# Performance work log

Hardware: AMD Instinct MI355X
Metric: run time of the kernel (lower is better)

## Reference

```python
import jax, jax.numpy as jnp
import numpy as np

DIM = 256
NUM_HEADS = 8
HEAD_DIM = DIM // NUM_HEADS


def setup_inputs() -> dict:
    key = jax.random.key(0)
    k1, k2, k3, k4 = jax.random.split(key, 4)
    B, C, H, W = 16, DIM, 64, 64
    x = jax.random.normal(k1, (B, C, H, W), dtype=jnp.float32)
    # 1x1 convs as dense weight matrices [out_ch, in_ch]
    Wqkv = jax.random.normal(k2, (3 * DIM, DIM), dtype=jnp.float32) * (DIM ** -0.5)
    Wproj = jax.random.normal(k3, (DIM, DIM), dtype=jnp.float32) * (DIM ** -0.5)
    bproj = jax.random.normal(k4, (DIM,), dtype=jnp.float32) * 0.01
    return {"x": x, "Wqkv": Wqkv, "Wproj": Wproj, "bproj": bproj}


def reference(x, Wqkv, Wproj, bproj):
    B, C, H, W = x.shape
    N = H * W
    hd = C // NUM_HEADS

    # qkv: 1x1 conv (no bias) == channel matmul
    qkv = jnp.einsum('oc,bchw->bohw', Wqkv, x)  # [B, 3C, H, W]
    q, k, v = jnp.split(qkv, 3, axis=1)

    def to_heads(t):
        # b (h d) x y -> b h (x y) d
        return t.reshape(B, NUM_HEADS, hd, N).transpose(0, 1, 3, 2)

    q, k, v = to_heads(q), to_heads(k), to_heads(v)  # [B, h, N, d]

    # linear attention feature map + per-token normalization over d
    q = jax.nn.elu(q) + 1.0
    k = jax.nn.elu(k) + 1.0
    q = q / jnp.sum(q, axis=-1, keepdims=True)
    k = k / jnp.sum(k, axis=-1, keepdims=True)

    kv = jnp.einsum('bhnd,bhne->bhde', k, v)   # [B, h, d, d]
    out = jnp.einsum('bhnd,bhde->bhne', q, kv)  # [B, h, N, d]

    # b h (x y) d -> b (h d) x y
    out = out.transpose(0, 1, 3, 2).reshape(B, C, H, W)

    # proj: 1x1 conv with bias; drop_path is identity in eval mode
    out = jnp.einsum('oc,bchw->bohw', Wproj, out) + bproj[None, :, None, None]
    return out + x
```

## Files before the change

### kernel.cpp

```cpp
#include <hip/hip_runtime.h>
#include <stdint.h>
#include <stddef.h>

#define DIM   256
#define NH    8
#define HD    32
#define BATCH 16
#define NTOK  4096

typedef __attribute__((ext_vector_type(8))) short short8;
typedef __attribute__((ext_vector_type(4))) float f32x4;

__device__ __forceinline__ unsigned short f2bf(float x){
  unsigned u = __float_as_uint(x);
  u += 0x7fffu + ((u >> 16) & 1u);
  return (unsigned short)(u >> 16);
}
__device__ __forceinline__ float elu1(float v){
  return (v > 0.f) ? (v + 1.f) : __expf(v);
}
__device__ __forceinline__ void gload_lds16(const void* g, void* lds){
  __builtin_amdgcn_global_load_lds(
      (const __attribute__((address_space(1))) unsigned int*)g,
      (__attribute__((address_space(3))) unsigned int*)lds, 16, 0, 0);
}

__global__ __launch_bounds__(256) void k_transpose_x(const float* __restrict__ x,
                                                     unsigned short* __restrict__ xt){
  __shared__ float tile[64][65];
  const int b = blockIdx.z, c0 = blockIdx.y * 64, n0 = blockIdx.x * 64;
  const float* xb = x + (size_t)b * DIM * NTOK;
  const int t = threadIdx.x;
  #pragma unroll
  for (int p = 0; p < 4; p++){
    int idx = t + p * 256;
    int row = idx >> 4;
    int col = (idx & 15) << 2;
    float4 v = *(const float4*)(xb + (size_t)(c0 + row) * NTOK + n0 + col);
    tile[row][col] = v.x; tile[row][col+1] = v.y; tile[row][col+2] = v.z; tile[row][col+3] = v.w;
  }
  __syncthreads();
  unsigned short* xtb = xt + (size_t)b * NTOK * DIM;
  #pragma unroll
  for (int p = 0; p < 4; p++){
    int idx = t + p * 256;
    int nl = idx >> 4;
    int cl = (idx & 15) << 2;
    ushort4 o;
    o.x = f2bf(tile[cl+0][nl]); o.y = f2bf(tile[cl+1][nl]);
    o.z = f2bf(tile[cl+2][nl]); o.w = f2bf(tile[cl+3][nl]);
    *(ushort4*)(xtb + (size_t)(n0 + nl) * DIM + c0 + cl) = o;
  }
}

__global__ __launch_bounds__(256) void k_convert_w(const float* __restrict__ wqkv,
                                                   unsigned short* __restrict__ wq_bf){
  int i = blockIdx.x * 256 + threadIdx.x;
  int row = i >> 6;
  int c4 = (i & 63) * 4;
  int dst;
  if (row < 256)      dst = row;
  else if (row < 512){ int p = (row - 256) >> 6; int s = (row - 256) & 63; dst = 256 + p*128 + s; }
  else               { int p = (row - 512) >> 6; int s = (row - 512) & 63; dst = 256 + p*128 + 64 + s; }
  float4 v = *(const float4*)(wqkv + (size_t)row * DIM + c4);
  ushort4 o = { f2bf(v.x), f2bf(v.y), f2bf(v.z), f2bf(v.w) };
  *(ushort4*)(wq_bf + (size_t)dst * DIM + c4) = o;
}

__global__ __launch_bounds__(512, 4) void k_qkv5(const unsigned short* __restrict__ wbf,
                                                 const unsigned short* __restrict__ xt,
                                                 unsigned short* __restrict__ qn,
                                                 float* __restrict__ kvp){
  __shared__ __align__(16) unsigned short sh[17408];
  unsigned short* As = sh;
  unsigned short* Bs = sh + 8192;
  const int t = threadIdx.x;
  const int w = t >> 6, l = t & 63;
  const int t16 = l & 15, quad = l >> 4;
  const int wm = w >> 1, wn = w & 1;
  const int bid = blockIdx.x;
  const int super = bid / 48;
  const int rem = bid - super * 48;
  const int m = rem >> 3, lx = rem & 7;
  const int g = super * 8 + lx;
  const int nt = g >> 4, b = g & 15;
  const int o0 = m * 128, n0 = nt * 128;
  const unsigned short* A = wbf;
  const unsigned short* B = xt + (size_t)b * NTOK * DIM;

  f32x4 acc[2][4];
  #pragma unroll
  for (int i = 0; i < 2; i++)
    #pragma unroll
    for (int j = 0; j < 4; j++){ acc[i][j][0]=0.f; acc[i][j][1]=0.f; acc[i][j][2]=0.f; acc[i][j][3]=0.f; }

  for (int k0 = 0; k0 < 256; k0 += 64){
    __syncthreads();
    #pragma unroll
    for (int s4 = 0; s4 < 4; s4++){
      int s = w * 4 + s4;
      int sl = s & 15;
      int tile = sl >> 1, kk = sl & 1;
      const unsigned short* src = (s < 16)
          ? (A + (size_t)(o0 + tile*16 + t16) * DIM + k0 + kk*32 + quad*8)
          : (B + (size_t)(n0 + tile*16 + t16) * DIM + k0 + kk*32 + quad*8);
      gload_lds16(src, sh + s * 512);
    }
    __syncthreads();
    #pragma unroll
    for (int kk = 0; kk < 2; kk++){
      short8 a[2], bb[4];
      #pragma unroll
      for (int i = 0; i < 2; i++) a[i]  = *(const short8*)(As + ((wm*2 + i)*2 + kk) * 512 + l * 8);
      #pragma unroll
      for (int j = 0; j < 4; j++) bb[j] = *(const short8*)(Bs + ((wn*4 + j)*2 + kk) * 512 + l * 8);
      #pragma unroll
      for (int i = 0; i < 2; i++)
        #pragma unroll
        for (int j = 0; j < 4; j++)
          acc[i][j] = __builtin_amdgcn_mfma_f32_16x16x32_bf16(a[i], bb[j], acc[i][j], 0, 0, 0);
    }
  }
  __syncthreads();

  const bool isQ = (o0 < 256);
  if (isQ || wm < 2){
    #pragma unroll
    for (int i = 0; i < 2; i++)
      #pragma unroll
      for (int j = 0; j < 4; j++)
        #pragma unroll
        for (int r = 0; r < 4; r++) acc[i][j][r] = elu1(acc[i][j][r]);
    float s[4];
    #pragma unroll
    for (int j = 0; j < 4; j++){
      float v = 0.f;
      #pragma unroll
      for (int i = 0; i < 2; i++)
        #pragma unroll
        for (int r = 0; r < 4; r++) v += acc[i][j][r];
      v += __shfl_xor(v, 16);
      v += __shfl_xor(v, 32);
      s[j] = 1.0f / v;
    }
    #pragma unroll
    for (int i = 0; i < 2; i++)
      #pragma unroll
      for (int j = 0; j < 4; j++){
        float inv = s[j];
        #pragma unroll
        for (int r = 0; r < 4; r++) acc[i][j][r] *= inv;
      }
  }

  if (isQ){
    #pragma unroll
    for (int i = 0; i < 2; i++)
      #pragma unroll
      for (int j = 0; j < 4; j++){
        int n_l = wn*64 + j*16 + t16;
        int o_l0 = wm*32 + i*16 + quad*4;
        ushort4 pk = { f2bf(acc[i][j][0]), f2bf(acc[i][j][1]),
                       f2bf(acc[i][j][2]), f2bf(acc[i][j][3]) };
        *(ushort4*)(sh + n_l*136 + o_l0) = pk;
      }
    __syncthreads();
    unsigned short* dst = qn + (size_t)b * NTOK * DIM;
    #pragma unroll
    for (int p = 0; p < 4; p++){
      int gg = t + p * 512;
      int n_l = gg >> 4, c = gg & 15;
      uint4 v = *(const uint4*)(sh + n_l*136 + c*8);
      *(uint4*)(dst + (size_t)(n0 + n_l) * DIM + o0 + c*8) = v;
    }
  } else {
    #pragma unroll
    for (int i = 0; i < 2; i++)
      #pragma unroll
      for (int j = 0; j < 4; j++){
        int n_l = wn*64 + j*16 + t16;
        #pragma unroll
        for (int r = 0; r < 4; r++){
          int o_l = wm*32 + i*16 + quad*4 + r;
          sh[o_l*136 + n_l] = f2bf(acc[i][j][r]);
        }
      }
    __syncthreads();
    const int p = (o0 >> 7) - 2;
    const int hl = w >> 2, dh = (w >> 1) & 1, eh = w & 1;
    f32x4 kvacc;
    kvacc[0]=0.f; kvacc[1]=0.f; kvacc[2]=0.f; kvacc[3]=0.f;
    const unsigned short* kbase = sh + (hl*32 + dh*16) * 136;
    const unsigned short* vbase = sh + (64 + hl*32 + eh*16) * 136;
    #pragma unroll
    for (int kk = 0; kk < 4; kk++){
      int nn = kk*32 + quad*8;
      short8 afrag = *(const short8*)(kbase + t16*136 + nn);
      short8 bfrag = *(const short8*)(vbase + t16*136 + nn);
      kvacc = __builtin_amdgcn_mfma_f32_16x16x32_bf16(afrag, bfrag, kvacc, 0, 0, 0);
    }
    float* dst = kvp + ((size_t)(b*8 + p*2 + hl) * 32 + nt) * 1024;
    #pragma unroll
    for (int r = 0; r < 4; r++)
      dst[(dh*16 + quad*4 + r)*32 + eh*16 + t16] = kvacc[r];
  }
}

__global__ __launch_bounds__(256) void k_M(const float* __restrict__ kvp,
                                           const float* __restrict__ wproj,
                                           unsigned short* __restrict__ M){
  __shared__ float kvL[1024];
  __shared__ float wpL[8192];
  const int t = threadIdx.x;
  const int h = blockIdx.x, b = blockIdx.y;
  const float* pbase = kvp + (size_t)((b*8 + h)*32) * 1024;
  {
    float4 a = {0.f,0.f,0.f,0.f};
    #pragma unroll
    for (int p = 0; p < 32; p++){
      float4 v = *(const float4*)(pbase + (size_t)p*1024 + t*4);
      a.x += v.x; a.y += v.y; a.z += v.z; a.w += v.w;
    }
    *(float4*)(kvL + t*4) = a;
  }
  #pragma unroll
  for (int p = 0; p < 8; p++){
    int idx = t + p * 256;
    int o = idx >> 3, e4 = idx & 7;
    *(float4*)(wpL + o*32 + e4*4) = *(const float4*)(wproj + (size_t)o * DIM + h*32 + e4*4);
  }
  __syncthreads();
  float wr[32];
  #pragma unroll
  for (int e = 0; e < 32; e++) wr[e] = wpL[t*32 + e];
  unsigned short md[32];
  #pragma unroll
  for (int d = 0; d < 32; d++){
    float a = 0.f;
    #pragma unroll
    for (int e = 0; e < 32; e++) a += wr[e] * kvL[d*32 + e];
    md[d] = f2bf(a);
  }
  unsigned short* dst = M + (size_t)b * 65536 + (size_t)t * DIM + h*32;
  #pragma unroll
  for (int q = 0; q < 4; q++) *(uint4*)(dst + q*8) = *(const uint4*)(md + q*8);
}

__global__ __launch_bounds__(512, 4) void k_out5(const unsigned short* __restrict__ M,
                                                 const unsigned short* __restrict__ qn,
                                                 const float* __restrict__ x,
                                                 const float* __restrict__ bproj,
                                                 float* __restrict__ out){
  __shared__ __align__(16) unsigned short As[8192];
  __shared__ __align__(16) unsigned short Bs[8192];
  const int t = threadIdx.x;
  const int w = t >> 6, l = t & 63;
  const int t16 = l & 15, quad = l >> 4;
  const int wm = w >> 1, wn = w & 1;
  const int bid = blockIdx.x;
  const int super = bid >> 4;
  const int rem = bid & 15;
  const int m = rem >> 3, lx = rem & 7;
  const int g = super * 8 + lx;
  const int nt = g >> 4, b = g & 15;
  const int o0 = m * 128, n0 = nt * 128;
  const unsigned short* A = qn + (size_t)b * NTOK * DIM;
  const unsigned short* Bm = M + (size_t)b * 65536;

  f32x4 acc[2][4];
  #pragma unroll
  for (int i = 0; i < 2; i++)
    #pragma unroll
    for (int j = 0; j < 4; j++){ acc[i][j][0]=0.f; acc[i][j][1]=0.f; acc[i][j][2]=0.f; acc[i][j][3]=0.f; }

  for (int k0 = 0; k0 < 256; k0 += 64){
    __syncthreads();
    #pragma unroll
    for (int s4 = 0; s4 < 4; s4++){
      int s = w * 4 + s4;
      int sl = s & 15;
      int tile = sl >> 1, kk = sl & 1;
      const unsigned short* src = (s < 16)
          ? (A  + (size_t)(n0 + tile*16 + t16) * DIM + k0 + kk*32 + quad*8)
          : (Bm + (size_t)(o0 + tile*16 + t16) * DIM + k0 + kk*32 + quad*8);
      gload_lds16(src, (s < 16) ? (As + sl * 512) : (Bs + sl * 512));
    }
    __syncthreads();
    #pragma unroll
    for (int kk = 0; kk < 2; kk++){
      short8 a[2], bb[4];
      #pragma unroll
      for (int i = 0; i < 2; i++) a[i]  = *(const short8*)(As + ((wm*2 + i)*2 + kk) * 512 + l * 8);
      #pragma unroll
      for (int j = 0; j < 4; j++) bb[j] = *(const short8*)(Bs + ((wn*4 + j)*2 + kk) * 512 + l * 8);
      #pragma unroll
      for (int i = 0; i < 2; i++)
        #pragma unroll
        for (int j = 0; j < 4; j++)
          acc[i][j] = __builtin_amdgcn_mfma_f32_16x16x32_bf16(a[i], bb[j], acc[i][j], 0, 0, 0);
    }
  }

  const float* xb = x + (size_t)b * DIM * NTOK;
  float* ob = out + (size_t)b * DIM * NTOK;
  #pragma unroll
  for (int j = 0; j < 4; j++){
    int o = o0 + wn*64 + j*16 + t16;
    float bias = bproj[o];
    #pragma unroll
    for (int i = 0; i < 2; i++){
      int n = n0 + wm*32 + i*16 + quad*4;
      float4 xv = *(const float4*)(xb + (size_t)o * NTOK + n);
      float4 res = { acc[i][j][0] + bias + xv.x,
                     acc[i][j][1] + bias + xv.y,
                     acc[i][j][2] + bias + xv.z,
                     acc[i][j][3] + bias + xv.w };
      *(float4*)(ob + (size_t)o * NTOK + n) = res;
    }
  }
}

extern "C" void kernel_launch(void* const* d_in, const int* in_sizes, int n_in,
                              void* d_out, int out_size, void* d_ws, size_t ws_size,
                              hipStream_t stream){
  const float* x     = (const float*)d_in[0];
  const float* wqkv  = (const float*)d_in[1];
  const float* wproj = (const float*)d_in[2];
  const float* bproj = (const float*)d_in[3];
  float* out = (float*)d_out;
  char* ws = (char*)d_ws;

  unsigned short* xt   = (unsigned short*)(ws);
  unsigned short* qn   = (unsigned short*)(ws + ((size_t)32 << 20));
  float* kvp           = (float*)(ws + ((size_t)64 << 20));
  unsigned short* M    = (unsigned short*)(ws + ((size_t)80 << 20));
  unsigned short* wqbf = (unsigned short*)(ws + ((size_t)82 << 20));

  k_transpose_x<<<dim3(64, 4, 16), 256, 0, stream>>>(x, xt);
  k_convert_w  <<<dim3(192), 256, 0, stream>>>(wqkv, wqbf);
  k_qkv5       <<<dim3(3072), 512, 0, stream>>>(wqbf, xt, qn, kvp);
  k_M          <<<dim3(8, 16), 256, 0, stream>>>(kvp, wproj, M);
  k_out5       <<<dim3(1024), 512, 0, stream>>>(M, qn, x, bproj, out);
}
```

Before: 230.9 us.

## Keep weight tile in registers and process two token tiles per qkv block

The qkv GEMM kernel now loads its full 128x256 weight slice into registers once, then streams two 128-token tiles of x through a double-buffered LDS pipeline using split vmcnt waits. This halves the grid, removes repeated weight loads, and overlaps global loads with MFMA work. The KV partial sums are accumulated across both token tiles in registers, so the kvp partials and the k_M reduction loop shrink from 32 to 16. The cost is heavier register use from the a_reg array and a larger LDS footprint, which may reduce occupancy.

```diff
diff --git a/kernel.cpp b/kernel.cpp
--- a/kernel.cpp
+++ b/kernel.cpp
@@ -67,13 +67,12 @@
   *(ushort4*)(wq_bf + (size_t)dst * DIM + c4) = o;
 }
 
-__global__ __launch_bounds__(512, 4) void k_qkv5(const unsigned short* __restrict__ wbf,
+__global__ __launch_bounds__(512, 4) void k_qkv6(const unsigned short* __restrict__ wbf,
                                                  const unsigned short* __restrict__ xt,
                                                  unsigned short* __restrict__ qn,
                                                  float* __restrict__ kvp){
-  __shared__ __align__(16) unsigned short sh[17408];
-  unsigned short* As = sh;
-  unsigned short* Bs = sh + 8192;
+  __shared__ __align__(16) unsigned short sh[33792];
+  unsigned short* bsh = sh + 16384;
   const int t = threadIdx.x;
   const int w = t >> 6, l = t & 63;
   const int t16 = l & 15, quad = l >> 4;
@@ -82,124 +81,161 @@
   const int super = bid / 48;
   const int rem = bid - super * 48;
   const int m = rem >> 3, lx = rem & 7;
-  const int g = super * 8 + lx;
-  const int nt = g >> 4, b = g & 15;
-  const int o0 = m * 128, n0 = nt * 128;
-  const unsigned short* A = wbf;
-  const unsigned short* B = xt + (size_t)b * NTOK * DIM;
+  const int chunk = super * 8 + lx;
+  const int b = chunk >> 4, nt2 = chunk & 15;
+  const int o0 = m * 128;
+  const bool isQ = (o0 < 256);
+  const unsigned short* Bb = xt + ((size_t)b * NTOK + (size_t)nt2 * 256) * DIM;
+  const int rowL = (w*16 + t16) * DIM + quad*8;
+
+  short8 a_reg[4][2][2];
+  #pragma unroll
+  for (int rp = 0; rp < 2; rp++){
+    const unsigned short* srcA = wbf + (size_t)o0 * DIM + rowL + rp*128;
+    gload_lds16(srcA,      sh +        (w*2+0)*512);
+    gload_lds16(srcA + 32, sh +        (w*2+1)*512);
+    gload_lds16(srcA + 64, sh + 8192 + (w*2+0)*512);
+    gload_lds16(srcA + 96, sh + 8192 + (w*2+1)*512);
+    asm volatile("s_waitcnt vmcnt(0)" ::: "memory");
+    __builtin_amdgcn_s_barrier();
+    #pragma unroll
+    for (int cc = 0; cc < 2; cc++)
+      #pragma unroll
+      for (int i = 0; i < 2; i++)
+        #pragma unroll
+        for (int kk = 0; kk < 2; kk++)
+          a_reg[rp*2+cc][i][kk] = *(const short8*)(sh + cc*8192 + ((wm*2+i)*2+kk)*512 + l*8);
+    asm volatile("s_waitcnt lgkmcnt(0)" ::: "memory");
+    __builtin_amdgcn_s_barrier();
+  }
+
+  gload_lds16(Bb + rowL,      sh +        (w*2+0)*512);
+  gload_lds16(Bb + rowL + 32, sh +        (w*2+1)*512);
+  gload_lds16(Bb + rowL + 64, sh + 8192 + (w*2+0)*512);
+  gload_lds16(Bb + rowL + 96, sh + 8192 + (w*2+1)*512);
 
   f32x4 acc[2][4];
   #pragma unroll
   for (int i = 0; i < 2; i++)
     #pragma unroll
     for (int j = 0; j < 4; j++){ acc[i][j][0]=0.f; acc[i][j][1]=0.f; acc[i][j][2]=0.f; acc[i][j][3]=0.f; }
-
-  for (int k0 = 0; k0 < 256; k0 += 64){
-    __syncthreads();
-    #pragma unroll
-    for (int s4 = 0; s4 < 4; s4++){
-      int s = w * 4 + s4;
-      int sl = s & 15;
-      int tile = sl >> 1, kk = sl & 1;
-      const unsigned short* src = (s < 16)
-          ? (A + (size_t)(o0 + tile*16 + t16) * DIM + k0 + kk*32 + quad*8)
-          : (B + (size_t)(n0 + tile*16 + t16) * DIM + k0 + kk*32 + quad*8);
-      gload_lds16(src, sh + s * 512);
-    }
-    __syncthreads();
+  f32x4 kvacc;
+  kvacc[0]=0.f; kvacc[1]=0.f; kvacc[2]=0.f; kvacc[3]=0.f;
+
+  #pragma unroll
+  for (int s = 0; s < 8; s++){
+    if (s < 7) { asm volatile("s_waitcnt vmcnt(2)" ::: "memory"); }
+    else       { asm volatile("s_waitcnt vmcnt(0)" ::: "memory"); }
+    __builtin_amdgcn_s_barrier();
+    const unsigned short* bufc = sh + (s & 1) * 8192;
     #pragma unroll
     for (int kk = 0; kk < 2; kk++){
-      short8 a[2], bb[4];
-      #pragma unroll
-      for (int i = 0; i < 2; i++) a[i]  = *(const short8*)(As + ((wm*2 + i)*2 + kk) * 512 + l * 8);
-      #pragma unroll
-      for (int j = 0; j < 4; j++) bb[j] = *(const short8*)(Bs + ((wn*4 + j)*2 + kk) * 512 + l * 8);
+      short8 bb[4];
+      #pragma unroll
+      for (int j = 0; j < 4; j++) bb[j] = *(const short8*)(bufc + ((wn*4+j)*2+kk)*512 + l*8);
       #pragma unroll
       for (int i = 0; i < 2; i++)
         #pragma unroll
         for (int j = 0; j < 4; j++)
-          acc[i][j] = __builtin_amdgcn_mfma_f32_16x16x32_bf16(a[i], bb[j], acc[i][j], 0, 0, 0);
-    }
-  }
-  __syncthreads();
-
-  const bool isQ = (o0 < 256);
-  if (isQ || wm < 2){
-    #pragma unroll
-    for (int i = 0; i < 2; i++)
-      #pragma unroll
-      for (int j = 0; j < 4; j++)
-        #pragma unroll
-        for (int r = 0; r < 4; r++) acc[i][j][r] = elu1(acc[i][j][r]);
-    float s[4];
-    #pragma unroll
-    for (int j = 0; j < 4; j++){
-      float v = 0.f;
-      #pragma unroll
-      for (int i = 0; i < 2; i++)
-        #pragma unroll
-        for (int r = 0; r < 4; r++) v += acc[i][j][r];
-      v += __shfl_xor(v, 16);
-      v += __shfl_xor(v, 32);
-      s[j] = 1.0f / v;
-    }
-    #pragma unroll
-    for (int i = 0; i < 2; i++)
-      #pragma unroll
-      for (int j = 0; j < 4; j++){
-        float inv = s[j];
-        #pragma unroll
-        for (int r = 0; r < 4; r++) acc[i][j][r] *= inv;
+          acc[i][j] = __builtin_amdgcn_mfma_f32_16x16x32_bf16(a_reg[s&3][i][kk], bb[j], acc[i][j], 0, 0, 0);
+    }
+    __builtin_amdgcn_s_barrier();
+    if (s < 6){
+      const int s2 = s + 2;
+      const unsigned short* src = Bb + (size_t)((s2 >> 2) * 128) * DIM + rowL + (s2 & 3) * 64;
+      unsigned short* db = sh + (s & 1) * 8192;
+      gload_lds16(src,      db + (w*2+0)*512);
+      gload_lds16(src + 32, db + (w*2+1)*512);
+    }
+    if ((s & 3) == 3){
+      const int n0 = (nt2*2 + (s >> 2)) * 128;
+      if (isQ || wm < 2){
+        #pragma unroll
+        for (int i = 0; i < 2; i++)
+          #pragma unroll
+          for (int j = 0; j < 4; j++)
+            #pragma unroll
+            for (int r = 0; r < 4; r++) acc[i][j][r] = elu1(acc[i][j][r]);
+        float sc[4];
+        #pragma unroll
+        for (int j = 0; j < 4; j++){
+          float v = 0.f;
+          #pragma unroll
+          for (int i = 0; i < 2; i++)
+            #pragma unroll
+            for (int r = 0; r < 4; r++) v += acc[i][j][r];
+          v += __shfl_xor(v, 16);
+          v += __shfl_xor(v, 32);
+          sc[j] = 1.0f / v;
+        }
+        #pragma unroll
+        for (int i = 0; i < 2; i++)
+          #pragma unroll
+          for (int j = 0; j < 4; j++){
+            float inv = sc[j];
+            #pragma unroll
+            for (int r = 0; r < 4; r++) acc[i][j][r] *= inv;
+          }
       }
-  }
-
-  if (isQ){
-    #pragma unroll
-    for (int i = 0; i < 2; i++)
-      #pragma unroll
-      for (int j = 0; j < 4; j++){
-        int n_l = wn*64 + j*16 + t16;
-        int o_l0 = wm*32 + i*16 + quad*4;
-        ushort4 pk = { f2bf(acc[i][j][0]), f2bf(acc[i][j][1]),
-                       f2bf(acc[i][j][2]), f2bf(acc[i][j][3]) };
-        *(ushort4*)(sh + n_l*136 + o_l0) = pk;
-      }
-    __syncthreads();
-    unsigned short* dst = qn + (size_t)b * NTOK * DIM;
-    #pragma unroll
-    for (int p = 0; p < 4; p++){
-      int gg = t + p * 512;
-      int n_l = gg >> 4, c = gg & 15;
-      uint4 v = *(const uint4*)(sh + n_l*136 + c*8);
-      *(uint4*)(dst + (size_t)(n0 + n_l) * DIM + o0 + c*8) = v;
-    }
-  } else {
-    #pragma unroll
-    for (int i = 0; i < 2; i++)
-      #pragma unroll
-      for (int j = 0; j < 4; j++){
-        int n_l = wn*64 + j*16 + t16;
-        #pragma unroll
-        for (int r = 0; r < 4; r++){
-          int o_l = wm*32 + i*16 + quad*4 + r;
-          sh[o_l*136 + n_l] = f2bf(acc[i][j][r]);
+      if (isQ){
+        #pragma unroll
+        for (int i = 0; i < 2; i++)
+          #pragma unroll
+          for (int j = 0; j < 4; j++){
+            int n_l = wn*64 + j*16 + t16;
+            int o_l0 = wm*32 + i*16 + quad*4;
+            ushort4 pk = { f2bf(acc[i][j][0]), f2bf(acc[i][j][1]),
+                           f2bf(acc[i][j][2]), f2bf(acc[i][j][3]) };
+            *(ushort4*)(bsh + n_l*136 + o_l0) = pk;
+          }
+        asm volatile("s_waitcnt lgkmcnt(0)" ::: "memory");
+        __builtin_amdgcn_s_barrier();
+        unsigned short* dst = qn + (size_t)b * NTOK * DIM;
+        #pragma unroll
+        for (int p2 = 0; p2 < 4; p2++){
+          int gg = t + p2 * 512;
+          int n_l = gg >> 4, c = gg & 15;
+          uint4 v = *(const uint4*)(bsh + n_l*136 + c*8);
+          *(uint4*)(dst + (size_t)(n0 + n_l) * DIM + o0 + c*8) = v;
+        }
+      } else {
+        #pragma unroll
+        for (int i = 0; i < 2; i++)
+          #pragma unroll
+          for (int j = 0; j < 4; j++){
+            int n_l = wn*64 + j*16 + t16;
+            #pragma unroll
+            for (int r = 0; r < 4; r++){
+              int o_l = wm*32 + i*16 + quad*4 + r;
+              bsh[o_l*136 + n_l] = f2bf(acc[i][j][r]);
+            }
+          }
+        asm volatile("s_waitcnt lgkmcnt(0)" ::: "memory");
+        __builtin_amdgcn_s_barrier();
+        const int hl = w >> 2, dh = (w >> 1) & 1, eh = w & 1;
+        const unsigned short* kbase = bsh + (hl*32 + dh*16) * 136;
+        const unsigned short* vbase = bsh + (64 + hl*32 + eh*16) * 136;
+        #pragma unroll
+        for (int kk2 = 0; kk2 < 4; kk2++){
+          int nn = kk2*32 + quad*8;
+          short8 afrag = *(const short8*)(kbase + t16*136 + nn);
+          short8 bfrag = *(const short8*)(vbase + t16*136 + nn);
+          kvacc = __builtin_amdgcn_mfma_f32_16x16x32_bf16(afrag, bfrag, kvacc, 0, 0, 0);
         }
       }
-    __syncthreads();
-    const int p = (o0 >> 7) - 2;
+      if (s == 3){
+        #pragma unroll
+        for (int i = 0; i < 2; i++)
+          #pragma unroll
+          for (int j = 0; j < 4; j++){ acc[i][j][0]=0.f; acc[i][j][1]=0.f; acc[i][j][2]=0.f; acc[i][j][3]=0.f; }
+      }
+    }
+  }
+
+  if (!isQ){
+    const int pp = (o0 >> 7) - 2;
     const int hl = w >> 2, dh = (w >> 1) & 1, eh = w & 1;
-    f32x4 kvacc;
-    kvacc[0]=0.f; kvacc[1]=0.f; kvacc[2]=0.f; kvacc[3]=0.f;
-    const unsigned short* kbase = sh + (hl*32 + dh*16) * 136;
-    const unsigned short* vbase = sh + (64 + hl*32 + eh*16) * 136;
-    #pragma unroll
-    for (int kk = 0; kk < 4; kk++){
-      int nn = kk*32 + quad*8;
-      short8 afrag = *(const short8*)(kbase + t16*136 + nn);
-      short8 bfrag = *(const short8*)(vbase + t16*136 + nn);
-      kvacc = __builtin_amdgcn_mfma_f32_16x16x32_bf16(afrag, bfrag, kvacc, 0, 0, 0);
-    }
-    float* dst = kvp + ((size_t)(b*8 + p*2 + hl) * 32 + nt) * 1024;
+    float* dst = kvp + ((size_t)((b*8 + pp*2 + hl) * 16 + nt2)) * 1024;
     #pragma unroll
     for (int r = 0; r < 4; r++)
       dst[(dh*16 + quad*4 + r)*32 + eh*16 + t16] = kvacc[r];
@@ -213,11 +249,11 @@
   __shared__ float wpL[8192];
   const int t = threadIdx.x;
   const int h = blockIdx.x, b = blockIdx.y;
-  const float* pbase = kvp + (size_t)((b*8 + h)*32) * 1024;
+  const float* pbase = kvp + (size_t)((b*8 + h) * 16) * 1024;
   {
     float4 a = {0.f,0.f,0.f,0.f};
     #pragma unroll
-    for (int p = 0; p < 32; p++){
+    for (int p = 0; p < 16; p++){
       float4 v = *(const float4*)(pbase + (size_t)p*1024 + t*4);
       a.x += v.x; a.y += v.y; a.z += v.z; a.w += v.w;
     }
@@ -338,7 +374,7 @@
 
   k_transpose_x<<<dim3(64, 4, 16), 256, 0, stream>>>(x, xt);
   k_convert_w  <<<dim3(192), 256, 0, stream>>>(wqkv, wqbf);
-  k_qkv5       <<<dim3(3072), 512, 0, stream>>>(wqbf, xt, qn, kvp);
+  k_qkv6       <<<dim3(1536), 512, 0, stream>>>(wqbf, xt, qn, kvp);
   k_M          <<<dim3(8, 16), 256, 0, stream>>>(kvp, wproj, M);
   k_out5       <<<dim3(1024), 512, 0, stream>>>(M, qn, x, bproj, out);
 }
```

Result: slower. 236.3 us (+2.3%).
